# Kernel tuning notes

Hardware: AMD Instinct MI355X
Metric: run time of the kernel (lower is better)

## Reference

```python
import jax, jax.numpy as jnp
import numpy as np

B = 512
C = 256
HEADS = 16
DH = 16
SIGMA = 1e-4  # GaussianNoise(0.0001)
LEAK = 0.2


def _axial_attn(x, Wq, Wkv, Wo, bo, axis):
    # x: [B, 8, 4, 5, C]; attend along `axis`, folding other dims into batch.
    xm = jnp.moveaxis(x, axis, -2)                      # [..., T, C]
    q = xm @ Wq                                          # [..., T, C]
    kv = xm @ Wkv                                        # [..., T, 2C]
    k, v = kv[..., :C], kv[..., C:]
    hshape = q.shape[:-1] + (HEADS, DH)
    q = q.reshape(hshape)
    k = k.reshape(hshape)
    v = v.reshape(hshape)
    dots = jnp.einsum('...thd,...shd->...hts', q, k) * (DH ** -0.5)
    attn = jax.nn.softmax(dots, axis=-1)
    o = jnp.einsum('...hts,...shd->...thd', attn, v).reshape(xm.shape)
    o = o @ Wo + bo
    return jnp.moveaxis(o, -2, axis)


def setup_inputs() -> dict:
    key = jax.random.key(0)
    ks = jax.random.split(key, 12)
    inp = {
        'x': jax.random.normal(ks[0], (B, 8, 4, 5), jnp.float32),
        'noise': jax.random.normal(ks[1], (B, 8, 4, 5, 1), jnp.float32),
        'rand': jax.random.uniform(ks[2], (B, 8, 4, 5, 1), jnp.float32),
        # encoder Linear(2, 256, bias=False), stored as [in, out]
        'W_enc': jax.random.normal(ks[3], (2, C), jnp.float32) * (2 ** -0.5),
        # axial positional embedding (sum of per-axis params == one full param)
        'pos_emb': jax.random.normal(ks[4], (8, 4, 5, C), jnp.float32) * 0.02,
        # 2 AxialAttention layers x 3 axes of SelfAttention params
        'Wq': jax.random.normal(ks[5], (2, 3, C, C), jnp.float32) * (C ** -0.5),
        'Wkv': jax.random.normal(ks[6], (2, 3, C, 2 * C), jnp.float32) * (C ** -0.5),
        'Wo': jax.random.normal(ks[7], (2, 3, C, C), jnp.float32) * (C ** -0.5),
        'bo': jnp.zeros((2, 3, C), jnp.float32),
        # decoder Linear(256, 1, bias=True)
        'Wd': jax.random.normal(ks[8], (C, 1), jnp.float32) * (C ** -0.5),
        'bd': jnp.zeros((1,), jnp.float32),
    }
    return inp


def reference(x, noise, rand, W_enc, pos_emb, Wq, Wkv, Wo, bo, Wd, bd):
    h = x[..., None] + SIGMA * noise                  # unsqueeze + GaussianNoise
    h = jnp.concatenate([h, rand], axis=-1)           # [B,8,4,5,2]
    h = jnp.tanh(h @ W_enc)                           # [B,8,4,5,256]
    h = h + pos_emb                                   # axial positional embedding
    for l in range(2):                                # two AxialAttention blocks
        h = (_axial_attn(h, Wq[l, 0], Wkv[l, 0], Wo[l, 0], bo[l, 0], 1)
             + _axial_attn(h, Wq[l, 1], Wkv[l, 1], Wo[l, 1], bo[l, 1], 2)
             + _axial_attn(h, Wq[l, 2], Wkv[l, 2], Wo[l, 2], bo[l, 2], 3))
        h = jnp.where(h >= 0, h, LEAK * h)            # LeakyReLU(0.2)
    out = jax.nn.sigmoid(h @ Wd + bd)                 # decoder Linear + Sigmoid
    return out[..., 0]                                # squeeze(-1) -> [B,8,4,5]
```

## Files before the change

### kernel.cpp

```cpp
#include <hip/hip_runtime.h>
#include <hip/hip_bf16.h>
#include <math.h>

#define NPOS 81920
#define CDIM 256
#define SIGMA 1e-4f
#define LEAK 0.2f

typedef __hip_bfloat16 bf16;
typedef __bf16 bf16x8 __attribute__((ext_vector_type(8)));
typedef float f32x4 __attribute__((ext_vector_type(4)));

__device__ __forceinline__ float bf2f(unsigned short u) {
    return __uint_as_float(((unsigned)u) << 16);
}
__device__ __forceinline__ unsigned short f2bfu(float f) {
    bf16 h = __float2bfloat16(f);
    return *reinterpret_cast<unsigned short*>(&h);
}

__global__ void encode_kernel(const float* __restrict__ x, const float* __restrict__ noise,
                              const float* __restrict__ rnd, const float* __restrict__ We,
                              const float* __restrict__ pe, bf16* __restrict__ H) {
    int p = blockIdx.x;
    int c = threadIdx.x;
    float a = x[p] + SIGMA * noise[p];
    float b = rnd[p];
    float z = a * We[c] + b * We[CDIM + c];
    z = fminf(15.f, fmaxf(-15.f, z));
    float e = __expf(2.f * z);
    float th = 1.f - 2.f / (e + 1.f);
    H[(size_t)p * CDIM + c] = __float2bfloat16(th + pe[(p % 160) * CDIM + c]);
}

__global__ void bias3_kernel(const float* __restrict__ bo, float* __restrict__ bsum) {
    int l = blockIdx.x, c = threadIdx.x;
    bsum[l * CDIM + c] = bo[l * 768 + c] + bo[l * 768 + 256 + c] + bo[l * 768 + 512 + c];
}

__global__ void pack_qkv_kernel(const float* __restrict__ Wq, const float* __restrict__ Wkv,
                                bf16* __restrict__ out) {
    int mat = blockIdx.x / 768;
    int n = blockIdx.x % 768;
    int k = threadIdx.x;
    float v = (n < 256) ? Wq[(size_t)mat * 65536 + (size_t)k * 256 + n]
                        : Wkv[(size_t)mat * 131072 + (size_t)k * 512 + (n - 256)];
    out[(size_t)blockIdx.x * 256 + k] = __float2bfloat16(v);
}
__global__ void pack_wo_kernel(const float* __restrict__ Wo, bf16* __restrict__ out) {
    int l = blockIdx.x / 256;
    int n = blockIdx.x % 256;
    int ck = threadIdx.x;
    for (int a = 0; a < 3; a++)
        out[(size_t)(l * 256 + n) * 768 + a * 256 + ck] =
            __float2bfloat16(Wo[(((size_t)(l * 3 + a)) * 256 + ck) * 256 + n]);
}

__global__ __launch_bounds__(256, 2) void step_kernel(
    const bf16* __restrict__ Hg, const bf16* __restrict__ Wqkv, bf16* __restrict__ QKV,
    const bf16* __restrict__ O, const bf16* __restrict__ WoTl, bf16* __restrict__ Hnw,
    const float* __restrict__ bias, int nW, int nMblk) {
    __shared__ __bf16 smem[32768];
    int tid = threadIdx.x;
    int wave = tid >> 6, lane = tid & 63;
    int quad = lane >> 4, m = lane & 15;

    if (blockIdx.x >= nW) {
        __bf16* As = smem;
        __bf16* Bs = smem + 8192;
        int bid = blockIdx.x - nW;
        int xcd = bid & 7, slot = bid >> 3;
        int g = slot / 9;
        int nb = slot - g * 9;
        int mb = xcd + 8 * g;
        int bm = mb * 128, bn = nb * 256;
        int wr = (wave >> 1) * 64, wc = (wave & 1) * 128;
        f32x4 acc[4][8] = {};

#define STAGE_G(buf, k0)                                                                       \
    {                                                                                          \
        _Pragma("unroll") for (int rep = 0; rep < 2; rep++) {                                  \
            int ch = rep * 256 + wave * 64 + lane;                                             \
            int row = ch >> 2, cc = ch & 3, gc = cc ^ ((row >> 1) & 3);                        \
            __builtin_amdgcn_global_load_lds(                                                  \
                (const __attribute__((address_space(1))) void*)(Hg + (size_t)(bm + row) * CDIM \
                                                                + (k0) + gc * 8),              \
                (__attribute__((address_space(3))) void*)(As + (buf) * 4096                    \
                                                          + (rep * 256 + wave * 64) * 8),      \
                16, 0, 0);                                                                     \
        }                                                                                      \
        _Pragma("unroll") for (int rep = 0; rep < 4; rep++) {                                  \
            int ch = rep * 256 + wave * 64 + lane;                                             \
            int row = ch >> 2, cc = ch & 3, gc = cc ^ ((row >> 1) & 3);                        \
            __builtin_amdgcn_global_load_lds(                                                  \
                (const __attribute__((address_space(1))) void*)(Wqkv + (size_t)(bn + row) * 256\
                                                                + (k0) + gc * 8),              \
                (__attribute__((address_space(3))) void*)(Bs + (buf) * 8192                    \
                                                          + (rep * 256 + wave * 64) * 8),      \
                16, 0, 0);                                                                     \
        }                                                                                      \
    }

        STAGE_G(0, 0);
#pragma unroll
        for (int it = 0; it < 8; it++) {
            __syncthreads();
            if (it < 7) STAGE_G((it + 1) & 1, (it + 1) * 32);
            const __bf16* Ab = As + (it & 1) * 4096;
            const __bf16* Bb = Bs + (it & 1) * 8192;
            bf16x8 af[4], bfr[8];
#pragma unroll
            for (int i = 0; i < 4; i++) {
                int r = wr + i * 16 + m;
                af[i] = *(const bf16x8*)(Ab + r * 32 + ((quad ^ ((r >> 1) & 3)) * 8));
            }
#pragma unroll
            for (int j = 0; j < 8; j++) {
                int r = wc + j * 16 + m;
                bfr[j] = *(const bf16x8*)(Bb + r * 32 + ((quad ^ ((r >> 1) & 3)) * 8));
            }
#pragma unroll
            for (int i = 0; i < 4; i++)
#pragma unroll
                for (int j = 0; j < 8; j++)
                    acc[i][j] = __builtin_amdgcn_mfma_f32_16x16x32_bf16(af[i], bfr[j], acc[i][j], 0, 0, 0);
        }
#undef STAGE_G

#pragma unroll
        for (int i = 0; i < 4; i++)
#pragma unroll
            for (int j = 0; j < 8; j++)
#pragma unroll
                for (int r = 0; r < 4; r++) {
                    int row = bm + wr + i * 16 + quad * 4 + r;
                    int col = bn + wc + j * 16 + m;
                    QKV[(size_t)row * 2304 + col] = __float2bfloat16(acc[i][j][r]);
                }
    } else {
        __bf16* As = smem;
        __bf16* Bs = smem + 16384;
        int bid = blockIdx.x;
        int xcd = bid & 7, slot = bid >> 3;
        int g = slot >> 1;
        int nb = slot & 1;
        int mb = xcd + 8 * g;
        int bm = mb * 128, bn = nb * 128;
        int wr = (wave >> 1) * 64, wc = (wave & 1) * 64;
        f32x4 acc[4][4] = {};

#define STAGE_W(buf, k0)                                                                       \
    {                                                                                          \
        _Pragma("unroll") for (int rep = 0; rep < 4; rep++) {                                  \
            int ch = rep * 256 + wave * 64 + lane;                                             \
            int row = ch >> 3, cc = ch & 7, gc = cc ^ (row & 7);                               \
            __builtin_amdgcn_global_load_lds(                                                  \
                (const __attribute__((address_space(1))) void*)(O + (size_t)(bm + row) * 768   \
                                                                + (k0) + gc * 8),              \
                (__attribute__((address_space(3))) void*)(As + (buf) * 8192                    \
                                                          + (rep * 256 + wave * 64) * 8),      \
                16, 0, 0);                                                                     \
        }                                                                                      \
        _Pragma("unroll") for (int rep = 0; rep < 4; rep++) {                                  \
            int ch = rep * 256 + wave * 64 + lane;                                             \
            int row = ch >> 3, cc = ch & 7, gc = cc ^ (row & 7);                               \
            __builtin_amdgcn_global_load_lds(                                                  \
                (const __attribute__((address_space(1))) void*)(WoTl + (size_t)(bn + row) * 768\
                                                                + (k0) + gc * 8),              \
                (__attribute__((address_space(3))) void*)(Bs + (buf) * 8192                    \
                                                          + (rep * 256 + wave * 64) * 8),      \
                16, 0, 0);                                                                     \
        }                                                                                      \
    }

        STAGE_W(0, 0);
#pragma unroll
        for (int it = 0; it < 12; it++) {
            __syncthreads();
            if (it < 11) STAGE_W((it + 1) & 1, (it + 1) * 64);
            const __bf16* Ab = As + (it & 1) * 8192;
            const __bf16* Bb = Bs + (it & 1) * 8192;
#pragma unroll
            for (int kk = 0; kk < 2; kk++) {
                bf16x8 af[4], bfr[4];
#pragma unroll
                for (int i = 0; i < 4; i++) {
                    int r = wr + i * 16 + m, cix = kk * 4 + quad;
                    af[i] = *(const bf16x8*)(Ab + r * 64 + ((cix ^ (r & 7)) * 8));
                }
#pragma unroll
                for (int j = 0; j < 4; j++) {
                    int r = wc + j * 16 + m, cix = kk * 4 + quad;
                    bfr[j] = *(const bf16x8*)(Bb + r * 64 + ((cix ^ (r & 7)) * 8));
                }
#pragma unroll
                for (int i = 0; i < 4; i++)
#pragma unroll
                    for (int j = 0; j < 4; j++)
                        acc[i][j] = __builtin_amdgcn_mfma_f32_16x16x32_bf16(af[i], bfr[j], acc[i][j], 0, 0, 0);
            }
        }
#undef STAGE_W

#pragma unroll
        for (int i = 0; i < 4; i++)
#pragma unroll
            for (int j = 0; j < 4; j++)
#pragma unroll
                for (int r = 0; r < 4; r++) {
                    int row = bm + wr + i * 16 + quad * 4 + r;
                    int col = bn + wc + j * 16 + m;
                    float v = acc[i][j][r] + bias[col];
                    v = v >= 0.f ? v : LEAK * v;
                    Hnw[(size_t)row * CDIM + col] = __float2bfloat16(v);
                }
    }
}

template <int AXIS>
__device__ __forceinline__ void attn_axis(const bf16* __restrict__ QKV, bf16* __restrict__ O,
                                          int seq, int lane) {
    constexpr int T      = (AXIS == 0) ? 8 : (AXIS == 1) ? 4 : 5;
    constexpr int STRIDE = (AXIS == 0) ? 20 : (AXIS == 1) ? 5 : 1;
    int base;
    if (AXIS == 0)      { int b = seq / 20, r = seq % 20; base = b * 160 + r; }
    else if (AXIS == 1) { int b = seq / 40, r = seq % 40; base = b * 160 + (r / 5) * 20 + (r % 5); }
    else                { int b = seq / 32, r = seq % 32; base = b * 160 + r * 5; }

    float q[T][4], k[T][4], v[T][4];
#pragma unroll
    for (int t = 0; t < T; t++) {
        const unsigned short* rowp =
            (const unsigned short*)QKV + (size_t)(base + t * STRIDE) * 2304 + AXIS * 768 + lane * 4;
        ushort4 qu = *(const ushort4*)(rowp);
        ushort4 ku = *(const ushort4*)(rowp + 256);
        ushort4 vu = *(const ushort4*)(rowp + 512);
        q[t][0] = bf2f(qu.x); q[t][1] = bf2f(qu.y); q[t][2] = bf2f(qu.z); q[t][3] = bf2f(qu.w);
        k[t][0] = bf2f(ku.x); k[t][1] = bf2f(ku.y); k[t][2] = bf2f(ku.z); k[t][3] = bf2f(ku.w);
        v[t][0] = bf2f(vu.x); v[t][1] = bf2f(vu.y); v[t][2] = bf2f(vu.z); v[t][3] = bf2f(vu.w);
    }

#pragma unroll
    for (int t = 0; t < T; t++) {
        float sc[T];
#pragma unroll
        for (int s = 0; s < T; s++) {
            float p = q[t][0] * k[s][0] + q[t][1] * k[s][1] + q[t][2] * k[s][2] + q[t][3] * k[s][3];
            p += __shfl_xor(p, 1);
            p += __shfl_xor(p, 2);
            sc[s] = p * 0.25f;
        }
        float mx = sc[0];
#pragma unroll
        for (int s = 1; s < T; s++) mx = fmaxf(mx, sc[s]);
        float sum = 0.f;
#pragma unroll
        for (int s = 0; s < T; s++) { sc[s] = __expf(sc[s] - mx); sum += sc[s]; }
        float inv = 1.f / sum;
        float o0 = 0.f, o1 = 0.f, o2 = 0.f, o3 = 0.f;
#pragma unroll
        for (int s = 0; s < T; s++) {
            o0 += sc[s] * v[s][0]; o1 += sc[s] * v[s][1];
            o2 += sc[s] * v[s][2]; o3 += sc[s] * v[s][3];
        }
        ushort4 st;
        st.x = f2bfu(o0 * inv); st.y = f2bfu(o1 * inv);
        st.z = f2bfu(o2 * inv); st.w = f2bfu(o3 * inv);
        *(ushort4*)((unsigned short*)O + (size_t)(base + t * STRIDE) * 768 + AXIS * 256 + lane * 4) = st;
    }
}

__global__ __launch_bounds__(256) void attn_all(const bf16* __restrict__ QKV,
                                                bf16* __restrict__ O, int n0, int n1) {
    int wave = threadIdx.x >> 6, lane = threadIdx.x & 63;
    int blk = blockIdx.x;
    if (blk < n0)            attn_axis<0>(QKV, O, blk * 4 + wave, lane);
    else if (blk < n0 + n1)  attn_axis<1>(QKV, O, (blk - n0) * 4 + wave, lane);
    else                     attn_axis<2>(QKV, O, (blk - n0 - n1) * 4 + wave, lane);
}

__global__ void decode_kernel(const bf16* __restrict__ H, const float* __restrict__ Wd,
                              const float* __restrict__ bd, float* __restrict__ out) {
    int tid = threadIdx.x;
    int pos = blockIdx.x * 4 + (tid >> 6);
    int lane = tid & 63;
    float acc = 0.f;
#pragma unroll
    for (int q = 0; q < 4; q++) {
        int c = lane + q * 64;
        acc += __bfloat162float(H[(size_t)pos * CDIM + c]) * Wd[c];
    }
#pragma unroll
    for (int off = 32; off > 0; off >>= 1) acc += __shfl_down(acc, off);
    if (lane == 0) out[pos] = 1.f / (1.f + __expf(-(acc + bd[0])));
}

extern "C" void kernel_launch(void* const* d_in, const int* in_sizes, int n_in,
                              void* d_out, int out_size, void* d_ws, size_t ws_size,
                              hipStream_t stream) {
    const float* x     = (const float*)d_in[0];
    const float* noise = (const float*)d_in[1];
    const float* rnd   = (const float*)d_in[2];
    const float* We    = (const float*)d_in[3];
    const float* pe    = (const float*)d_in[4];
    const float* Wq    = (const float*)d_in[5];
    const float* Wkv   = (const float*)d_in[6];
    const float* Wo    = (const float*)d_in[7];
    const float* bo    = (const float*)d_in[8];
    const float* Wd    = (const float*)d_in[9];
    const float* bd    = (const float*)d_in[10];
    float* out = (float*)d_out;

    bf16* H0    = (bf16*)d_ws;
    bf16* H1    = H0 + (size_t)NPOS * CDIM;
    bf16* WqkvT = H1 + (size_t)NPOS * CDIM;
    bf16* WoT   = WqkvT + (size_t)2 * 2304 * 256;
    float* bsum = (float*)(WoT + (size_t)2 * 256 * 768);
    bf16* QKV   = (bf16*)(bsum + 512);

    size_t fixed = ((size_t)2 * NPOS * CDIM + (size_t)2 * 2304 * 256 + (size_t)2 * 256 * 768) * 2
                   + 512 * 4;
    int c = 4;
    while (c < 64 && fixed + (size_t)(NPOS / c) * (2304 + 768) * 2 > ws_size) c <<= 1;
    int mc = NPOS / c;
    bf16* O = QKV + (size_t)mc * 2304;
    bf16* Hbuf[3] = { H0, H1, H0 };

    pack_qkv_kernel<<<6 * 768, 256, 0, stream>>>(Wq, Wkv, WqkvT);
    pack_wo_kernel<<<2 * 256, 256, 0, stream>>>(Wo, WoT);
    bias3_kernel<<<2, 256, 0, stream>>>(bo, bsum);
    encode_kernel<<<NPOS, 256, 0, stream>>>(x, noise, rnd, We, pe, H0);

    int nMblk = mc / 128;
    int n0 = (mc / 160) * 20 / 4, n1 = (mc / 160) * 40 / 4, n2 = (mc / 160) * 32 / 4;
    int TT = 2 * c;

    for (int t = 0; t <= TT; t++) {
        int gG = (t < TT) ? nMblk * 9 : 0;
        int gW = (t >= 1) ? nMblk * 2 : 0;
        const bf16 *Hg = nullptr, *Wq_ = nullptr;
        if (gG) {
            int lg = t / c, cg = t % c;
            Hg = Hbuf[lg] + (size_t)cg * mc * CDIM;
            Wq_ = WqkvT + (size_t)lg * 2304 * 256;
        }
        const bf16* WoTl = nullptr; bf16* Hnw = nullptr; const float* bs = nullptr;
        if (gW) {
            int tw = t - 1, lw = tw / c, cw = tw % c;
            WoTl = WoT + (size_t)lw * 256 * 768;
            Hnw = Hbuf[lw + 1] + (size_t)cw * mc * CDIM;
            bs = bsum + lw * CDIM;
        }
        step_kernel<<<gG + gW, 256, 0, stream>>>(Hg, Wq_, QKV, O, WoTl, Hnw, bs, gW, nMblk);
        if (t < TT) attn_all<<<n0 + n1 + n2, 256, 0, stream>>>(QKV, O, n0, n1);
    }

    decode_kernel<<<NPOS / 4, 256, 0, stream>>>(Hbuf[2], Wd, bd, out);
}
```

Before: 687.2 us.

## Fuse attention into step kernel as a three-stage software pipeline with double buffers

Removes the separate attention launch and runs attention for chunk t-1 inside the same launch as the QKV GEMM for chunk t and the output projection for chunk t-2. QKV and O buffers are double-buffered so the stages can overlap, and attention and GEMM work units are interleaved across blocks in groups of 8 to balance XCDs. This halves the launch count and lets the memory-bound attention overlap the compute-bound GEMMs. The cost is a larger workspace, which can push toward smaller chunks, plus an extra pipeline step.

Result: no change. 692.5 us (+0.8%).

```diff
diff --git a/kernel.cpp b/kernel.cpp
--- a/kernel.cpp
+++ b/kernel.cpp
@@ -56,19 +56,86 @@
             __float2bfloat16(Wo[(((size_t)(l * 3 + a)) * 256 + ck) * 256 + n]);
 }
 
+template <int AXIS>
+__device__ __forceinline__ void attn_axis(const bf16* __restrict__ QKV, bf16* __restrict__ O,
+                                          int seq, int lane) {
+    constexpr int T      = (AXIS == 0) ? 8 : (AXIS == 1) ? 4 : 5;
+    constexpr int STRIDE = (AXIS == 0) ? 20 : (AXIS == 1) ? 5 : 1;
+    int base;
+    if (AXIS == 0)      { int b = seq / 20, r = seq % 20; base = b * 160 + r; }
+    else if (AXIS == 1) { int b = seq / 40, r = seq % 40; base = b * 160 + (r / 5) * 20 + (r % 5); }
+    else                { int b = seq / 32, r = seq % 32; base = b * 160 + r * 5; }
+
+    float q[T][4], k[T][4], v[T][4];
+#pragma unroll
+    for (int t = 0; t < T; t++) {
+        const unsigned short* rowp =
+            (const unsigned short*)QKV + (size_t)(base + t * STRIDE) * 2304 + AXIS * 768 + lane * 4;
+        ushort4 qu = *(const ushort4*)(rowp);
+        ushort4 ku = *(const ushort4*)(rowp + 256);
+        ushort4 vu = *(const ushort4*)(rowp + 512);
+        q[t][0] = bf2f(qu.x); q[t][1] = bf2f(qu.y); q[t][2] = bf2f(qu.z); q[t][3] = bf2f(qu.w);
+        k[t][0] = bf2f(ku.x); k[t][1] = bf2f(ku.y); k[t][2] = bf2f(ku.z); k[t][3] = bf2f(ku.w);
+        v[t][0] = bf2f(vu.x); v[t][1] = bf2f(vu.y); v[t][2] = bf2f(vu.z); v[t][3] = bf2f(vu.w);
+    }
+
+#pragma unroll
+    for (int t = 0; t < T; t++) {
+        float sc[T];
+#pragma unroll
+        for (int s = 0; s < T; s++) {
+            float p = q[t][0] * k[s][0] + q[t][1] * k[s][1] + q[t][2] * k[s][2] + q[t][3] * k[s][3];
+            p += __shfl_xor(p, 1);
+            p += __shfl_xor(p, 2);
+            sc[s] = p * 0.25f;
+        }
+        float mx = sc[0];
+#pragma unroll
+        for (int s = 1; s < T; s++) mx = fmaxf(mx, sc[s]);
+        float sum = 0.f;
+#pragma unroll
+        for (int s = 0; s < T; s++) { sc[s] = __expf(sc[s] - mx); sum += sc[s]; }
+        float inv = 1.f / sum;
+        float o0 = 0.f, o1 = 0.f, o2 = 0.f, o3 = 0.f;
+#pragma unroll
+        for (int s = 0; s < T; s++) {
+            o0 += sc[s] * v[s][0]; o1 += sc[s] * v[s][1];
+            o2 += sc[s] * v[s][2]; o3 += sc[s] * v[s][3];
+        }
+        ushort4 st;
+        st.x = f2bfu(o0 * inv); st.y = f2bfu(o1 * inv);
+        st.z = f2bfu(o2 * inv); st.w = f2bfu(o3 * inv);
+        *(ushort4*)((unsigned short*)O + (size_t)(base + t * STRIDE) * 768 + AXIS * 256 + lane * 4) = st;
+    }
+}
+
 __global__ __launch_bounds__(256, 2) void step_kernel(
     const bf16* __restrict__ Hg, const bf16* __restrict__ Wqkv, bf16* __restrict__ QKV,
     const bf16* __restrict__ O, const bf16* __restrict__ WoTl, bf16* __restrict__ Hnw,
-    const float* __restrict__ bias, int nW, int nMblk) {
+    const float* __restrict__ bias,
+    const bf16* __restrict__ QKVr, bf16* __restrict__ Oa,
+    int nWu, int nGu, int nAu, int n0, int n1) {
     __shared__ __bf16 smem[32768];
     int tid = threadIdx.x;
     int wave = tid >> 6, lane = tid & 63;
     int quad = lane >> 4, m = lane & 15;
-
-    if (blockIdx.x >= nW) {
+    int uid = blockIdx.x >> 3, l8 = blockIdx.x & 7;
+
+    if (uid >= nWu) {
+        int rem = uid - nWu;
+        int tot = nGu + nAu;
+        int au = rem * nAu / tot;
+        bool isA = ((rem + 1) * nAu / tot) > au;
+        if (isA) {
+            int blk = au * 8 + l8;
+            if (blk < n0)            attn_axis<0>(QKVr, Oa, blk * 4 + wave, lane);
+            else if (blk < n0 + n1)  attn_axis<1>(QKVr, Oa, (blk - n0) * 4 + wave, lane);
+            else                     attn_axis<2>(QKVr, Oa, (blk - n0 - n1) * 4 + wave, lane);
+            return;
+        }
         __bf16* As = smem;
         __bf16* Bs = smem + 8192;
-        int bid = blockIdx.x - nW;
+        int bid = (rem - au) * 8 + l8;
         int xcd = bid & 7, slot = bid >> 3;
         int g = slot / 9;
         int nb = slot - g * 9;
@@ -217,68 +284,6 @@
     }
 }
 
-template <int AXIS>
-__device__ __forceinline__ void attn_axis(const bf16* __restrict__ QKV, bf16* __restrict__ O,
-                                          int seq, int lane) {
-    constexpr int T      = (AXIS == 0) ? 8 : (AXIS == 1) ? 4 : 5;
-    constexpr int STRIDE = (AXIS == 0) ? 20 : (AXIS == 1) ? 5 : 1;
-    int base;
-    if (AXIS == 0)      { int b = seq / 20, r = seq % 20; base = b * 160 + r; }
-    else if (AXIS == 1) { int b = seq / 40, r = seq % 40; base = b * 160 + (r / 5) * 20 + (r % 5); }
-    else                { int b = seq / 32, r = seq % 32; base = b * 160 + r * 5; }
-
-    float q[T][4], k[T][4], v[T][4];
-#pragma unroll
-    for (int t = 0; t < T; t++) {
-        const unsigned short* rowp =
-            (const unsigned short*)QKV + (size_t)(base + t * STRIDE) * 2304 + AXIS * 768 + lane * 4;
-        ushort4 qu = *(const ushort4*)(rowp);
-        ushort4 ku = *(const ushort4*)(rowp + 256);
-        ushort4 vu = *(const ushort4*)(rowp + 512);
-        q[t][0] = bf2f(qu.x); q[t][1] = bf2f(qu.y); q[t][2] = bf2f(qu.z); q[t][3] = bf2f(qu.w);
-        k[t][0] = bf2f(ku.x); k[t][1] = bf2f(ku.y); k[t][2] = bf2f(ku.z); k[t][3] = bf2f(ku.w);
-        v[t][0] = bf2f(vu.x); v[t][1] = bf2f(vu.y); v[t][2] = bf2f(vu.z); v[t][3] = bf2f(vu.w);
-    }
-
-#pragma unroll
-    for (int t = 0; t < T; t++) {
-        float sc[T];
-#pragma unroll
-        for (int s = 0; s < T; s++) {
-            float p = q[t][0] * k[s][0] + q[t][1] * k[s][1] + q[t][2] * k[s][2] + q[t][3] * k[s][3];
-            p += __shfl_xor(p, 1);
-            p += __shfl_xor(p, 2);
-            sc[s] = p * 0.25f;
-        }
-        float mx = sc[0];
-#pragma unroll
-        for (int s = 1; s < T; s++) mx = fmaxf(mx, sc[s]);
-        float sum = 0.f;
-#pragma unroll
-        for (int s = 0; s < T; s++) { sc[s] = __expf(sc[s] - mx); sum += sc[s]; }
-        float inv = 1.f / sum;
-        float o0 = 0.f, o1 = 0.f, o2 = 0.f, o3 = 0.f;
-#pragma unroll
-        for (int s = 0; s < T; s++) {
-            o0 += sc[s] * v[s][0]; o1 += sc[s] * v[s][1];
-            o2 += sc[s] * v[s][2]; o3 += sc[s] * v[s][3];
-        }
-        ushort4 st;
-        st.x = f2bfu(o0 * inv); st.y = f2bfu(o1 * inv);
-        st.z = f2bfu(o2 * inv); st.w = f2bfu(o3 * inv);
-        *(ushort4*)((unsigned short*)O + (size_t)(base + t * STRIDE) * 768 + AXIS * 256 + lane * 4) = st;
-    }
-}
-
-__global__ __launch_bounds__(256) void attn_all(const bf16* __restrict__ QKV,
-                                                bf16* __restrict__ O, int n0, int n1) {
-    int wave = threadIdx.x >> 6, lane = threadIdx.x & 63;
-    int blk = blockIdx.x;
-    if (blk < n0)            attn_axis<0>(QKV, O, blk * 4 + wave, lane);
-    else if (blk < n0 + n1)  attn_axis<1>(QKV, O, (blk - n0) * 4 + wave, lane);
-    else                     attn_axis<2>(QKV, O, (blk - n0 - n1) * 4 + wave, lane);
-}
-
 __global__ void decode_kernel(const bf16* __restrict__ H, const float* __restrict__ Wd,
                               const float* __restrict__ bd, float* __restrict__ out) {
     int tid = threadIdx.x;
@@ -316,14 +321,16 @@
     bf16* WqkvT = H1 + (size_t)NPOS * CDIM;
     bf16* WoT   = WqkvT + (size_t)2 * 2304 * 256;
     float* bsum = (float*)(WoT + (size_t)2 * 256 * 768);
-    bf16* QKV   = (bf16*)(bsum + 512);
+    bf16* QKV0  = (bf16*)(bsum + 512);
 
     size_t fixed = ((size_t)2 * NPOS * CDIM + (size_t)2 * 2304 * 256 + (size_t)2 * 256 * 768) * 2
                    + 512 * 4;
     int c = 4;
-    while (c < 64 && fixed + (size_t)(NPOS / c) * (2304 + 768) * 2 > ws_size) c <<= 1;
+    while (c < 64 && fixed + (size_t)(NPOS / c) * (2304 + 768) * 2 * 2 > ws_size) c <<= 1;
     int mc = NPOS / c;
-    bf16* O = QKV + (size_t)mc * 2304;
+    bf16* QKV1 = QKV0 + (size_t)mc * 2304;
+    bf16* O0   = QKV1 + (size_t)mc * 2304;
+    bf16* O1   = O0 + (size_t)mc * 768;
     bf16* Hbuf[3] = { H0, H1, H0 };
 
     pack_qkv_kernel<<<6 * 768, 256, 0, stream>>>(Wq, Wkv, WqkvT);
@@ -332,27 +339,40 @@
     encode_kernel<<<NPOS, 256, 0, stream>>>(x, noise, rnd, We, pe, H0);
 
     int nMblk = mc / 128;
-    int n0 = (mc / 160) * 20 / 4, n1 = (mc / 160) * 40 / 4, n2 = (mc / 160) * 32 / 4;
+    int cells = mc / 160;
+    int n0 = cells * 20 / 4, n1 = cells * 40 / 4, n2 = cells * 32 / 4;
+    int nA = n0 + n1 + n2;
     int TT = 2 * c;
 
-    for (int t = 0; t <= TT; t++) {
-        int gG = (t < TT) ? nMblk * 9 : 0;
-        int gW = (t >= 1) ? nMblk * 2 : 0;
-        const bf16 *Hg = nullptr, *Wq_ = nullptr;
-        if (gG) {
+    for (int t = 0; t <= TT + 1; t++) {
+        int nGu = (t < TT) ? (nMblk * 9) >> 3 : 0;
+        int nAu = (t >= 1 && t <= TT) ? nA >> 3 : 0;
+        int nWu = (t >= 2) ? (nMblk * 2) >> 3 : 0;
+
+        const bf16 *HgP = nullptr, *WqP = nullptr; bf16* QKVw = nullptr;
+        if (nGu) {
             int lg = t / c, cg = t % c;
-            Hg = Hbuf[lg] + (size_t)cg * mc * CDIM;
-            Wq_ = WqkvT + (size_t)lg * 2304 * 256;
-        }
-        const bf16* WoTl = nullptr; bf16* Hnw = nullptr; const float* bs = nullptr;
-        if (gW) {
-            int tw = t - 1, lw = tw / c, cw = tw % c;
+            HgP  = Hbuf[lg] + (size_t)cg * mc * CDIM;
+            WqP  = WqkvT + (size_t)lg * 2304 * 256;
+            QKVw = (t & 1) ? QKV1 : QKV0;
+        }
+        const bf16* QKVr = nullptr; bf16* Oaw = nullptr;
+        if (nAu) {
+            int ta = t - 1;
+            QKVr = (ta & 1) ? QKV1 : QKV0;
+            Oaw  = (ta & 1) ? O1 : O0;
+        }
+        const bf16* Ord = nullptr; const bf16* WoTl = nullptr;
+        bf16* Hnw = nullptr; const float* bs = nullptr;
+        if (nWu) {
+            int tw = t - 2, lw = tw / c, cw = tw % c;
+            Ord  = (tw & 1) ? O1 : O0;
             WoTl = WoT + (size_t)lw * 256 * 768;
-            Hnw = Hbuf[lw + 1] + (size_t)cw * mc * CDIM;
-            bs = bsum + lw * CDIM;
-        }
-        step_kernel<<<gG + gW, 256, 0, stream>>>(Hg, Wq_, QKV, O, WoTl, Hnw, bs, gW, nMblk);
-        if (t < TT) attn_all<<<n0 + n1 + n2, 256, 0, stream>>>(QKV, O, n0, n1);
+            Hnw  = Hbuf[lw + 1] + (size_t)cw * mc * CDIM;
+            bs   = bsum + lw * CDIM;
+        }
+        step_kernel<<<(nWu + nGu + nAu) * 8, 256, 0, stream>>>(
+            HgP, WqP, QKVw, Ord, WoTl, Hnw, bs, QKVr, Oaw, nWu, nGu, nAu, n0, n1);
     }
 
     decode_kernel<<<NPOS / 4, 256, 0, stream>>>(Hbuf[2], Wd, bd, out);
```

## Fuse QKV projection with axial attention per cell, drop QKV buffer

Applied to the files above, without the earlier changes.

Replaces the separate QKV GEMM plus attention kernel with a fused block that loads one 160-position cell of H into LDS, computes Q/K/V for one axis and four heads at a time with MFMA, stages them in shared memory, and runs the per-head softmax attention there. The O buffer is double-buffered so the Wo GEMM of the previous chunk overlaps with the fused work of the next. This removes the large QKV global round-trip and one launch per step, and halves the chunk count. In exchange it uses more LDS and registers, uses small tiles (10x3 MFMA per wave per k-step), and reads B fragments straight from global memory with no reuse across blocks.

After: 1.339 ms. 94.8% more time.

```diff
diff --git a/kernel.cpp b/kernel.cpp
--- a/kernel.cpp
+++ b/kernel.cpp
@@ -56,87 +56,127 @@
             __float2bfloat16(Wo[(((size_t)(l * 3 + a)) * 256 + ck) * 256 + n]);
 }
 
+template <int AXIS>
+__device__ __forceinline__ void ga_attn_phase(const unsigned short* __restrict__ us,
+                                              bf16* __restrict__ Oa, int cell, int hg,
+                                              int wave, int lane) {
+    constexpr int T      = (AXIS == 0) ? 8 : (AXIS == 1) ? 4 : 5;
+    constexpr int STRIDE = (AXIS == 0) ? 20 : (AXIS == 1) ? 5 : 1;
+    constexpr int NS     = (AXIS == 0) ? 20 : (AXIS == 1) ? 40 : 32;
+    int quad = lane >> 4, c = lane & 15;
+    for (int s = wave; s < NS; s += 4) {
+        int base_r;
+        if (AXIS == 0)      base_r = s;
+        else if (AXIS == 1) base_r = (s / 5) * 20 + (s % 5);
+        else                base_r = (s / 4) * 20 + (s % 4) * 5;
+        float q[T], k[T], v[T];
+#pragma unroll
+        for (int t = 0; t < T; t++) {
+            int row = base_r + t * STRIDE;
+            int ub = row * 200 + quad * 48 + c;
+            q[t] = bf2f(us[ub]);
+            k[t] = bf2f(us[ub + 16]);
+            v[t] = bf2f(us[ub + 32]);
+        }
+#pragma unroll
+        for (int t = 0; t < T; t++) {
+            float sc[T];
+#pragma unroll
+            for (int s2 = 0; s2 < T; s2++) {
+                float p = q[t] * k[s2];
+                p += __shfl_xor(p, 1);
+                p += __shfl_xor(p, 2);
+                p += __shfl_xor(p, 4);
+                p += __shfl_xor(p, 8);
+                sc[s2] = p * 0.25f;
+            }
+            float mx = sc[0];
+#pragma unroll
+            for (int s2 = 1; s2 < T; s2++) mx = fmaxf(mx, sc[s2]);
+            float sum = 0.f;
+#pragma unroll
+            for (int s2 = 0; s2 < T; s2++) { sc[s2] = __expf(sc[s2] - mx); sum += sc[s2]; }
+            float inv = 1.f / sum;
+            float o = 0.f;
+#pragma unroll
+            for (int s2 = 0; s2 < T; s2++) o += sc[s2] * v[s2];
+            int row = base_r + t * STRIDE;
+            ((unsigned short*)Oa)[(size_t)(cell * 160 + row) * 768 + AXIS * 256 + hg * 64 + lane] =
+                f2bfu(o * inv);
+        }
+    }
+}
+
 __global__ __launch_bounds__(256, 2) void step_kernel(
-    const bf16* __restrict__ Hg, const bf16* __restrict__ Wqkv, bf16* __restrict__ QKV,
-    const bf16* __restrict__ O, const bf16* __restrict__ WoTl, bf16* __restrict__ Hnw,
-    const float* __restrict__ bias, int nW, int nMblk) {
-    __shared__ __bf16 smem[32768];
+    const bf16* __restrict__ Hg, const bf16* __restrict__ Wqkv, bf16* __restrict__ Oa,
+    const bf16* __restrict__ Ow, const bf16* __restrict__ WoTl, bf16* __restrict__ Hnw,
+    const float* __restrict__ bias, int nWb, int cells) {
+    __shared__ __bf16 smem[40960];
     int tid = threadIdx.x;
     int wave = tid >> 6, lane = tid & 63;
     int quad = lane >> 4, m = lane & 15;
 
-    if (blockIdx.x >= nW) {
-        __bf16* As = smem;
-        __bf16* Bs = smem + 8192;
-        int bid = blockIdx.x - nW;
-        int xcd = bid & 7, slot = bid >> 3;
-        int g = slot / 9;
-        int nb = slot - g * 9;
-        int mb = xcd + 8 * g;
-        int bm = mb * 128, bn = nb * 256;
-        int wr = (wave >> 1) * 64, wc = (wave & 1) * 128;
-        f32x4 acc[4][8] = {};
-
-#define STAGE_G(buf, k0)                                                                       \
-    {                                                                                          \
-        _Pragma("unroll") for (int rep = 0; rep < 2; rep++) {                                  \
-            int ch = rep * 256 + wave * 64 + lane;                                             \
-            int row = ch >> 2, cc = ch & 3, gc = cc ^ ((row >> 1) & 3);                        \
-            __builtin_amdgcn_global_load_lds(                                                  \
-                (const __attribute__((address_space(1))) void*)(Hg + (size_t)(bm + row) * CDIM \
-                                                                + (k0) + gc * 8),              \
-                (__attribute__((address_space(3))) void*)(As + (buf) * 4096                    \
-                                                          + (rep * 256 + wave * 64) * 8),      \
-                16, 0, 0);                                                                     \
-        }                                                                                      \
-        _Pragma("unroll") for (int rep = 0; rep < 4; rep++) {                                  \
-            int ch = rep * 256 + wave * 64 + lane;                                             \
-            int row = ch >> 2, cc = ch & 3, gc = cc ^ ((row >> 1) & 3);                        \
-            __builtin_amdgcn_global_load_lds(                                                  \
-                (const __attribute__((address_space(1))) void*)(Wqkv + (size_t)(bn + row) * 256\
-                                                                + (k0) + gc * 8),              \
-                (__attribute__((address_space(3))) void*)(Bs + (buf) * 8192                    \
-                                                          + (rep * 256 + wave * 64) * 8),      \
-                16, 0, 0);                                                                     \
-        }                                                                                      \
-    }
-
-        STAGE_G(0, 0);
-#pragma unroll
-        for (int it = 0; it < 8; it++) {
-            __syncthreads();
-            if (it < 7) STAGE_G((it + 1) & 1, (it + 1) * 32);
-            const __bf16* Ab = As + (it & 1) * 4096;
-            const __bf16* Bb = Bs + (it & 1) * 8192;
-            bf16x8 af[4], bfr[8];
-#pragma unroll
-            for (int i = 0; i < 4; i++) {
-                int r = wr + i * 16 + m;
-                af[i] = *(const bf16x8*)(Ab + r * 32 + ((quad ^ ((r >> 1) & 3)) * 8));
+    if (blockIdx.x >= nWb) {
+        int bid2 = blockIdx.x - nWb;
+        int cell = bid2 % cells;
+        int axis = bid2 / cells;
+        const bf16* Hc = Hg + (size_t)cell * 160 * CDIM;
+        unsigned short* us = (unsigned short*)smem;
+
+#pragma unroll 1
+        for (int hg = 0; hg < 4; hg++) {
+#pragma unroll
+            for (int rr = 0; rr < 20; rr++) {
+                int rd = rr * 8 + (tid >> 5);
+                int sd = tid & 31;
+                int sl = sd ^ ((rd >> 1) & 7);
+                __builtin_amdgcn_global_load_lds(
+                    (const __attribute__((address_space(1))) void*)(Hc + (size_t)rd * CDIM + sl * 8),
+                    (__attribute__((address_space(3))) void*)(smem + rd * 256 + sd * 8), 16, 0, 0);
             }
-#pragma unroll
-            for (int j = 0; j < 8; j++) {
-                int r = wc + j * 16 + m;
-                bfr[j] = *(const bf16x8*)(Bb + r * 32 + ((quad ^ ((r >> 1) & 3)) * 8));
+            __syncthreads();
+
+            int h = hg * 4 + wave;
+            f32x4 acc[10][3] = {};
+#pragma unroll
+            for (int kk = 0; kk < 8; kk++) {
+                bf16x8 bfrag[3];
+#pragma unroll
+                for (int p = 0; p < 3; p++)
+                    bfrag[p] = *(const bf16x8*)(Wqkv +
+                        (size_t)(axis * 768 + p * 256 + h * 16 + m) * 256 + kk * 32 + quad * 8);
+                bf16x8 afr[10];
+#pragma unroll
+                for (int mf = 0; mf < 10; mf++) {
+                    int row = mf * 16 + m;
+                    afr[mf] = *(const bf16x8*)(smem + row * 256 +
+                                               (((kk * 4 + quad) ^ ((row >> 1) & 7)) * 8));
+                }
+#pragma unroll
+                for (int mf = 0; mf < 10; mf++)
+#pragma unroll
+                    for (int p = 0; p < 3; p++)
+                        acc[mf][p] = __builtin_amdgcn_mfma_f32_16x16x32_bf16(afr[mf], bfrag[p],
+                                                                             acc[mf][p], 0, 0, 0);
             }
-#pragma unroll
-            for (int i = 0; i < 4; i++)
-#pragma unroll
-                for (int j = 0; j < 8; j++)
-                    acc[i][j] = __builtin_amdgcn_mfma_f32_16x16x32_bf16(af[i], bfr[j], acc[i][j], 0, 0, 0);
-        }
-#undef STAGE_G
-
-#pragma unroll
-        for (int i = 0; i < 4; i++)
-#pragma unroll
-            for (int j = 0; j < 8; j++)
-#pragma unroll
-                for (int r = 0; r < 4; r++) {
-                    int row = bm + wr + i * 16 + quad * 4 + r;
-                    int col = bn + wc + j * 16 + m;
-                    QKV[(size_t)row * 2304 + col] = __float2bfloat16(acc[i][j][r]);
-                }
+            __syncthreads();
+
+#pragma unroll
+            for (int mf = 0; mf < 10; mf++)
+#pragma unroll
+                for (int p = 0; p < 3; p++)
+#pragma unroll
+                    for (int r2 = 0; r2 < 4; r2++) {
+                        int row = mf * 16 + quad * 4 + r2;
+                        us[row * 200 + wave * 48 + p * 16 + m] = f2bfu(acc[mf][p][r2]);
+                    }
+            __syncthreads();
+
+            if (axis == 0)      ga_attn_phase<0>(us, Oa, cell, hg, wave, lane);
+            else if (axis == 1) ga_attn_phase<1>(us, Oa, cell, hg, wave, lane);
+            else                ga_attn_phase<2>(us, Oa, cell, hg, wave, lane);
+            __syncthreads();
+        }
     } else {
         __bf16* As = smem;
         __bf16* Bs = smem + 16384;
@@ -155,7 +195,7 @@
             int ch = rep * 256 + wave * 64 + lane;                                             \
             int row = ch >> 3, cc = ch & 7, gc = cc ^ (row & 7);                               \
             __builtin_amdgcn_global_load_lds(                                                  \
-                (const __attribute__((address_space(1))) void*)(O + (size_t)(bm + row) * 768   \
+                (const __attribute__((address_space(1))) void*)(Ow + (size_t)(bm + row) * 768  \
                                                                 + (k0) + gc * 8),              \
                 (__attribute__((address_space(3))) void*)(As + (buf) * 8192                    \
                                                           + (rep * 256 + wave * 64) * 8),      \
@@ -217,68 +257,6 @@
     }
 }
 
-template <int AXIS>
-__device__ __forceinline__ void attn_axis(const bf16* __restrict__ QKV, bf16* __restrict__ O,
-                                          int seq, int lane) {
-    constexpr int T      = (AXIS == 0) ? 8 : (AXIS == 1) ? 4 : 5;
-    constexpr int STRIDE = (AXIS == 0) ? 20 : (AXIS == 1) ? 5 : 1;
-    int base;
-    if (AXIS == 0)      { int b = seq / 20, r = seq % 20; base = b * 160 + r; }
-    else if (AXIS == 1) { int b = seq / 40, r = seq % 40; base = b * 160 + (r / 5) * 20 + (r % 5); }
-    else                { int b = seq / 32, r = seq % 32; base = b * 160 + r * 5; }
-
-    float q[T][4], k[T][4], v[T][4];
-#pragma unroll
-    for (int t = 0; t < T; t++) {
-        const unsigned short* rowp =
-            (const unsigned short*)QKV + (size_t)(base + t * STRIDE) * 2304 + AXIS * 768 + lane * 4;
-        ushort4 qu = *(const ushort4*)(rowp);
-        ushort4 ku = *(const ushort4*)(rowp + 256);
-        ushort4 vu = *(const ushort4*)(rowp + 512);
-        q[t][0] = bf2f(qu.x); q[t][1] = bf2f(qu.y); q[t][2] = bf2f(qu.z); q[t][3] = bf2f(qu.w);
-        k[t][0] = bf2f(ku.x); k[t][1] = bf2f(ku.y); k[t][2] = bf2f(ku.z); k[t][3] = bf2f(ku.w);
-        v[t][0] = bf2f(vu.x); v[t][1] = bf2f(vu.y); v[t][2] = bf2f(vu.z); v[t][3] = bf2f(vu.w);
-    }
-
-#pragma unroll
-    for (int t = 0; t < T; t++) {
-        float sc[T];
-#pragma unroll
-        for (int s = 0; s < T; s++) {
-            float p = q[t][0] * k[s][0] + q[t][1] * k[s][1] + q[t][2] * k[s][2] + q[t][3] * k[s][3];
-            p += __shfl_xor(p, 1);
-            p += __shfl_xor(p, 2);
-            sc[s] = p * 0.25f;
-        }
-        float mx = sc[0];
-#pragma unroll
-        for (int s = 1; s < T; s++) mx = fmaxf(mx, sc[s]);
-        float sum = 0.f;
-#pragma unroll
-        for (int s = 0; s < T; s++) { sc[s] = __expf(sc[s] - mx); sum += sc[s]; }
-        float inv = 1.f / sum;
-        float o0 = 0.f, o1 = 0.f, o2 = 0.f, o3 = 0.f;
-#pragma unroll
-        for (int s = 0; s < T; s++) {
-            o0 += sc[s] * v[s][0]; o1 += sc[s] * v[s][1];
-            o2 += sc[s] * v[s][2]; o3 += sc[s] * v[s][3];
-        }
-        ushort4 st;
-        st.x = f2bfu(o0 * inv); st.y = f2bfu(o1 * inv);
-        st.z = f2bfu(o2 * inv); st.w = f2bfu(o3 * inv);
-        *(ushort4*)((unsigned short*)O + (size_t)(base + t * STRIDE) * 768 + AXIS * 256 + lane * 4) = st;
-    }
-}
-
-__global__ __launch_bounds__(256) void attn_all(const bf16* __restrict__ QKV,
-                                                bf16* __restrict__ O, int n0, int n1) {
-    int wave = threadIdx.x >> 6, lane = threadIdx.x & 63;
-    int blk = blockIdx.x;
-    if (blk < n0)            attn_axis<0>(QKV, O, blk * 4 + wave, lane);
-    else if (blk < n0 + n1)  attn_axis<1>(QKV, O, (blk - n0) * 4 + wave, lane);
-    else                     attn_axis<2>(QKV, O, (blk - n0 - n1) * 4 + wave, lane);
-}
-
 __global__ void decode_kernel(const bf16* __restrict__ H, const float* __restrict__ Wd,
                               const float* __restrict__ bd, float* __restrict__ out) {
     int tid = threadIdx.x;
@@ -316,14 +294,14 @@
     bf16* WqkvT = H1 + (size_t)NPOS * CDIM;
     bf16* WoT   = WqkvT + (size_t)2 * 2304 * 256;
     float* bsum = (float*)(WoT + (size_t)2 * 256 * 768);
-    bf16* QKV   = (bf16*)(bsum + 512);
+    bf16* O0    = (bf16*)(bsum + 512);
 
     size_t fixed = ((size_t)2 * NPOS * CDIM + (size_t)2 * 2304 * 256 + (size_t)2 * 256 * 768) * 2
                    + 512 * 4;
-    int c = 4;
-    while (c < 64 && fixed + (size_t)(NPOS / c) * (2304 + 768) * 2 > ws_size) c <<= 1;
+    int c = 2;
+    while (c < 64 && fixed + (size_t)2 * (NPOS / c) * 768 * 2 > ws_size) c <<= 1;
     int mc = NPOS / c;
-    bf16* O = QKV + (size_t)mc * 2304;
+    bf16* O1 = O0 + (size_t)mc * 768;
     bf16* Hbuf[3] = { H0, H1, H0 };
 
     pack_qkv_kernel<<<6 * 768, 256, 0, stream>>>(Wq, Wkv, WqkvT);
@@ -332,27 +310,30 @@
     encode_kernel<<<NPOS, 256, 0, stream>>>(x, noise, rnd, We, pe, H0);
 
     int nMblk = mc / 128;
-    int n0 = (mc / 160) * 20 / 4, n1 = (mc / 160) * 40 / 4, n2 = (mc / 160) * 32 / 4;
+    int cells = mc / 160;
     int TT = 2 * c;
 
     for (int t = 0; t <= TT; t++) {
-        int gG = (t < TT) ? nMblk * 9 : 0;
-        int gW = (t >= 1) ? nMblk * 2 : 0;
-        const bf16 *Hg = nullptr, *Wq_ = nullptr;
-        if (gG) {
+        int nGA = (t < TT) ? cells * 3 : 0;
+        int nWb = (t >= 1) ? nMblk * 2 : 0;
+
+        const bf16 *HgP = nullptr, *WqP = nullptr; bf16* Oaw = nullptr;
+        if (nGA) {
             int lg = t / c, cg = t % c;
-            Hg = Hbuf[lg] + (size_t)cg * mc * CDIM;
-            Wq_ = WqkvT + (size_t)lg * 2304 * 256;
-        }
-        const bf16* WoTl = nullptr; bf16* Hnw = nullptr; const float* bs = nullptr;
-        if (gW) {
+            HgP = Hbuf[lg] + (size_t)cg * mc * CDIM;
+            WqP = WqkvT + (size_t)lg * 2304 * 256;
+            Oaw = (t & 1) ? O1 : O0;
+        }
+        const bf16* Ord = nullptr; const bf16* WoTl = nullptr;
+        bf16* Hnw = nullptr; const float* bs = nullptr;
+        if (nWb) {
             int tw = t - 1, lw = tw / c, cw = tw % c;
+            Ord  = (tw & 1) ? O1 : O0;
             WoTl = WoT + (size_t)lw * 256 * 768;
-            Hnw = Hbuf[lw + 1] + (size_t)cw * mc * CDIM;
-            bs = bsum + lw * CDIM;
-        }
-        step_kernel<<<gG + gW, 256, 0, stream>>>(Hg, Wq_, QKV, O, WoTl, Hnw, bs, gW, nMblk);
-        if (t < TT) attn_all<<<n0 + n1 + n2, 256, 0, stream>>>(QKV, O, n0, n1);
+            Hnw  = Hbuf[lw + 1] + (size_t)cw * mc * CDIM;
+            bs   = bsum + lw * CDIM;
+        }
+        step_kernel<<<nWb + nGA, 256, 0, stream>>>(HgP, WqP, Oaw, Ord, WoTl, Hnw, bs, nWb, cells);
     }
 
     decode_kernel<<<NPOS / 4, 256, 0, stream>>>(Hbuf[2], Wd, bd, out);
```
